# Kernel optimization log

Hardware: AMD Instinct MI355X
Metric: run time of the kernel (lower is better)

## Reference

```python
import jax, jax.numpy as jnp
import numpy as np

N = 100000   # nodes
E = 1600000  # edges
IN, HID, OUT = 128, 256, 64


def _glorot(key, shape):
    fan_in, fan_out = shape[1], shape[0]
    lim = (6.0 / (fan_in + fan_out)) ** 0.5
    return jax.random.uniform(key, shape, jnp.float32, -lim, lim)


def setup_inputs() -> dict:
    key = jax.random.key(0)
    ks = jax.random.split(key, 8)
    x = jax.random.normal(ks[0], (N, IN), jnp.float32)
    edge_index = jax.random.randint(ks[1], (2, E), 0, N, jnp.int64)
    # SAGEConv params: lin_l (neighbor path, has bias), lin_r (root path, no bias)
    return {
        "x": x,
        "edge_index": edge_index,
        "W1_l": _glorot(ks[2], (HID, IN)),
        "b1": jnp.zeros((HID,), jnp.float32),
        "W1_r": _glorot(ks[3], (HID, IN)),
        "W2_l": _glorot(ks[4], (OUT, HID)),
        "b2": jnp.zeros((OUT,), jnp.float32),
        "W2_r": _glorot(ks[5], (OUT, HID)),
    }


def _sage_conv(x, src, dst, W_l, b, W_r):
    # mean aggregation of neighbor features at destination nodes
    msg = x[src]                                             # [E, d] gather
    agg = jax.ops.segment_sum(msg, dst, num_segments=N)      # [N, d]
    cnt = jax.ops.segment_sum(jnp.ones((src.shape[0],), jnp.float32), dst,
                              num_segments=N)                # [N]
    mean = agg / jnp.maximum(cnt, 1.0)[:, None]
    return mean @ W_l.T + b + x @ W_r.T


def reference(x, edge_index, W1_l, b1, W1_r, W2_l, b2, W2_r):
    src, dst = edge_index[0], edge_index[1]
    h = jax.nn.relu(_sage_conv(x, src, dst, W1_l, b1, W1_r))
    # dropout is identity in eval mode
    return _sage_conv(h, src, dst, W2_l, b2, W2_r)
```

## Files before the change

### kernel.cpp

```cpp
#include <hip/hip_runtime.h>
#include <hip/hip_bf16.h>

#define NNODE 100000
#define NEDGE 1600000
#define NBBLK 512
#define CHUNK (NEDGE / NBBLK)
#define NB2 ((NNODE + 1023) >> 10)

typedef __attribute__((ext_vector_type(8))) short bf16x8;
typedef __attribute__((ext_vector_type(4))) float f32x4;

__device__ __forceinline__ unsigned short f2bf(float f){
  unsigned u = __float_as_uint(f);
  u += 0x7fffu + ((u >> 16) & 1u);
  return (unsigned short)(u >> 16);
}
__device__ __forceinline__ unsigned pk2(float a, float b){
  return (unsigned)f2bf(a) | ((unsigned)f2bf(b) << 16);
}
__device__ __forceinline__ float bflo(unsigned v){ return __uint_as_float(v << 16); }
__device__ __forceinline__ float bfhi(unsigned v){ return __uint_as_float(v & 0xffff0000u); }

__global__ __launch_bounds__(256) void k_hist(const int* __restrict__ dst,
                                              unsigned* __restrict__ gh){
  __shared__ unsigned h[NB2];
  for (int t = threadIdx.x; t < NB2; t += 256) h[t] = 0;
  __syncthreads();
  int base = blockIdx.x * CHUNK;
  for (int j = threadIdx.x; j < CHUNK; j += 256)
    atomicAdd(&h[dst[base + j] >> 10], 1u);
  __syncthreads();
  for (int t = threadIdx.x; t < NB2; t += 256) gh[blockIdx.x * NB2 + t] = h[t];
}

__global__ __launch_bounds__(512) void k_scan512(const unsigned* __restrict__ gh,
                                                 unsigned* __restrict__ gbase,
                                                 unsigned* __restrict__ btot){
  int b = blockIdx.x, t = threadIdx.x;
  int lane = t & 63, wv = t >> 6;
  unsigned v = gh[t * NB2 + b];
  unsigned s = v;
  #pragma unroll
  for (int off = 1; off < 64; off <<= 1){
    unsigned u = __shfl_up(s, off, 64);
    if (lane >= off) s += u;
  }
  __shared__ unsigned wsum[8];
  if (lane == 63) wsum[wv] = s;
  __syncthreads();
  unsigned woff = 0;
  for (int w = 0; w < wv; ++w) woff += wsum[w];
  gbase[t * NB2 + b] = woff + s - v;
  if (t == 511) btot[b] = woff + s;
}

__global__ __launch_bounds__(128) void k_scanb(const unsigned* __restrict__ btot,
                                               unsigned* __restrict__ bbase,
                                               unsigned* __restrict__ rowptr){
  __shared__ unsigned buf[128];
  int tid = threadIdx.x;
  unsigned v = (tid < NB2) ? btot[tid] : 0u;
  buf[tid] = v;
  __syncthreads();
  #pragma unroll
  for (int off = 1; off < 128; off <<= 1){
    unsigned t = (tid >= off) ? buf[tid - off] : 0u;
    __syncthreads();
    buf[tid] += t;
    __syncthreads();
  }
  if (tid < NB2) bbase[tid] = buf[tid] - v;
  if (tid == 0){ bbase[NB2] = NEDGE; rowptr[NNODE] = NEDGE; }
}

__global__ __launch_bounds__(256) void k_binscat(const int* __restrict__ src,
                                                 const int* __restrict__ dst,
                                                 const unsigned* __restrict__ gbase,
                                                 const unsigned* __restrict__ bbase,
                                                 unsigned* __restrict__ pairs){
  __shared__ unsigned cur[NB2];
  for (int t = threadIdx.x; t < NB2; t += 256)
    cur[t] = bbase[t] + gbase[blockIdx.x * NB2 + t];
  __syncthreads();
  int base = blockIdx.x * CHUNK;
  for (int j = threadIdx.x; j < CHUNK; j += 256){
    int s = src[base + j], d = dst[base + j];
    unsigned p = atomicAdd(&cur[d >> 10], 1u);
    pairs[p] = ((unsigned)s << 10) | (unsigned)(d & 1023);
  }
}

__global__ __launch_bounds__(1024) void k_buildcsr(const unsigned* __restrict__ bbase,
                                                   const unsigned* __restrict__ pairs,
                                                   unsigned* __restrict__ rowptr,
                                                   unsigned* __restrict__ col){
  __shared__ unsigned hist[1024];
  __shared__ unsigned wsum[16];
  const int b = blockIdx.x, tid = threadIdx.x;
  const int lane = tid & 63, wv = tid >> 6;
  const unsigned e0 = bbase[b], e1 = bbase[b + 1];
  const int nb0 = b << 10;
  hist[tid] = 0;
  __syncthreads();
  for (unsigned j = e0 + tid; j < e1; j += 1024)
    atomicAdd(&hist[pairs[j] & 1023u], 1u);
  __syncthreads();
  unsigned v = hist[tid];
  unsigned s = v;
  #pragma unroll
  for (int off = 1; off < 64; off <<= 1){
    unsigned u = __shfl_up(s, off, 64);
    if (lane >= off) s += u;
  }
  if (lane == 63) wsum[wv] = s;
  __syncthreads();
  unsigned woff = 0;
  for (int w = 0; w < wv; ++w) woff += wsum[w];
  unsigned gpos = e0 + woff + s - v;
  if (nb0 + tid < NNODE) rowptr[nb0 + tid] = gpos;
  __syncthreads();
  hist[tid] = gpos;
  __syncthreads();
  for (unsigned j = e0 + tid; j < e1; j += 1024){
    unsigned e = pairs[j];
    unsigned p = atomicAdd(&hist[e & 1023u], 1u);
    col[p] = e >> 10;
  }
}

__global__ void k_xcvt(const float* __restrict__ x, unsigned* __restrict__ A1u){
  int i = blockIdx.x * 256 + threadIdx.x;
  if (i >= NNODE * 32) return;
  float4 v = ((const float4*)x)[i];
  int e = i * 4;
  int row = e >> 7, c = e & 127;
  unsigned* d = A1u + (size_t)row * 128 + 64 + (c >> 1);
  d[0] = pk2(v.x, v.y);
  d[1] = pk2(v.z, v.w);
}

__global__ void k_wcvt1(const float* __restrict__ W1l, const float* __restrict__ W1r,
                        unsigned short* __restrict__ Bwt1){
  int i = blockIdx.x * 256 + threadIdx.x;
  if (i >= 256 * 256) return;
  int n = i >> 8, k = i & 255;
  float v = (k < 128) ? W1l[n * 128 + k] : W1r[n * 128 + (k - 128)];
  Bwt1[i] = f2bf(v);
}

__global__ void k_wcvt2(const float* __restrict__ W2l, const float* __restrict__ W2r,
                        unsigned short* __restrict__ Bwt2){
  int i = blockIdx.x * 256 + threadIdx.x;
  if (i >= 128 * 256) return;
  int n = i >> 8, k = i & 255;
  float v = (n < 64) ? W2l[n * 256 + k] : W2r[(n - 64) * 256 + k];
  Bwt2[i] = f2bf(v);
}

__global__ __launch_bounds__(256) void k_agg1(const unsigned* __restrict__ rowptr,
                                              const unsigned* __restrict__ col,
                                              unsigned* __restrict__ A1u){
  int gw = (blockIdx.x * 256 + threadIdx.x) >> 6;
  int lane = threadIdx.x & 63;
  if (gw >= NNODE) return;
  unsigned s0 = rowptr[gw], s1 = rowptr[gw + 1];
  float ax = 0.f, ay = 0.f;
  unsigned j = s0;
  for (; j + 3 < s1; j += 4){
    unsigned c0 = col[j], c1 = col[j+1], c2 = col[j+2], c3 = col[j+3];
    unsigned v0 = A1u[(size_t)c0 * 128 + 64 + lane];
    unsigned v1 = A1u[(size_t)c1 * 128 + 64 + lane];
    unsigned v2 = A1u[(size_t)c2 * 128 + 64 + lane];
    unsigned v3 = A1u[(size_t)c3 * 128 + 64 + lane];
    ax += bflo(v0) + bflo(v1) + bflo(v2) + bflo(v3);
    ay += bfhi(v0) + bfhi(v1) + bfhi(v2) + bfhi(v3);
  }
  for (; j < s1; ++j){
    unsigned v = A1u[(size_t)col[j] * 128 + 64 + lane];
    ax += bflo(v); ay += bfhi(v);
  }
  float inv = 1.f / fmaxf((float)(s1 - s0), 1.f);
  A1u[(size_t)gw * 128 + lane] = pk2(ax * inv, ay * inv);
}

template<int BN, bool RELU, bool BIAS>
__global__ __launch_bounds__(256) void k_gemm(const unsigned short* __restrict__ A,
                                              const unsigned short* __restrict__ B,
                                              const float* __restrict__ bias,
                                              unsigned short* __restrict__ C,
                                              int nrows){
  constexpr int NF = BN / 64;
  __shared__ unsigned short a_t[64 * 64];
  __shared__ unsigned short b_t[BN * 64];
  const int tid = threadIdx.x, wave = tid >> 6, lane = tid & 63;
  const int row0 = blockIdx.x * 64;
  char* ab = (char*)a_t;
  char* bb = (char*)b_t;

  f32x4 acc[4][NF];
  #pragma unroll
  for (int m = 0; m < 4; ++m)
    #pragma unroll
    for (int n = 0; n < NF; ++n)
      acc[m][n] = (f32x4){0.f, 0.f, 0.f, 0.f};

  for (int kt = 0; kt < 4; ++kt){
    {
      int r = tid >> 2;
      int gr = row0 + r; if (gr > nrows - 1) gr = nrows - 1;
      const uint4* s4 = (const uint4*)(A + (size_t)gr * 256 + kt * 64);
      int c0 = (tid & 3) * 2;
      uint4 v0 = s4[c0], v1 = s4[c0 + 1];
      *(uint4*)(ab + r * 128 + ((c0 * 16) ^ ((r & 7) << 4))) = v0;
      *(uint4*)(ab + r * 128 + (((c0 + 1) * 16) ^ ((r & 7) << 4))) = v1;
    }
    {
      constexpr int CPT = BN / 32;
      #pragma unroll
      for (int c = 0; c < CPT; ++c){
        int gc = tid * CPT + c;
        int n = gc >> 3, ck = gc & 7;
        uint4 v = ((const uint4*)(B + (size_t)n * 256 + kt * 64))[ck];
        *(uint4*)(bb + n * 128 + ((ck * 16) ^ ((n & 7) << 4))) = v;
      }
    }
    __syncthreads();
    #pragma unroll
    for (int kk = 0; kk < 2; ++kk){
      int k2 = (kk * 32 + ((lane >> 4) * 8)) * 2;
      bf16x8 af[4];
      #pragma unroll
      for (int m = 0; m < 4; ++m){
        int rr = m * 16 + (lane & 15);
        af[m] = *(const bf16x8*)(ab + rr * 128 + (k2 ^ ((rr & 7) << 4)));
      }
      #pragma unroll
      for (int n = 0; n < NF; ++n){
        int cc = wave * (16 * NF) + n * 16 + (lane & 15);
        bf16x8 bfv = *(const bf16x8*)(bb + cc * 128 + (k2 ^ ((cc & 7) << 4)));
        #pragma unroll
        for (int m = 0; m < 4; ++m)
          acc[m][n] = __builtin_amdgcn_mfma_f32_16x16x32_bf16(af[m], bfv, acc[m][n], 0, 0, 0);
      }
    }
    __syncthreads();
  }
  #pragma unroll
  for (int m = 0; m < 4; ++m){
    int rbase = row0 + m * 16 + ((lane >> 4) << 2);
    #pragma unroll
    for (int r = 0; r < 4; ++r){
      if (rbase + r < nrows){
        #pragma unroll
        for (int n = 0; n < NF; ++n){
          int cc = wave * (16 * NF) + n * 16 + (lane & 15);
          float v = acc[m][n][r];
          if (BIAS) v += bias[cc];
          if (RELU) v = fmaxf(v, 0.f);
          C[(size_t)(rbase + r) * BN + cc] = f2bf(v);
        }
      }
    }
  }
}

__global__ __launch_bounds__(256) void k_agg2(const unsigned* __restrict__ rowptr,
                                              const unsigned* __restrict__ col,
                                              const unsigned short* __restrict__ zr,
                                              const float* __restrict__ b2,
                                              float* __restrict__ out){
  int t = blockIdx.x * 256 + threadIdx.x;
  int node = t >> 4, gl = t & 15;
  if (node >= NNODE) return;
  unsigned s0 = rowptr[node], s1 = rowptr[node + 1];
  float a0 = 0.f, a1 = 0.f, a2 = 0.f, a3 = 0.f;
  unsigned j = s0;
  for (; j + 3 < s1; j += 4){
    unsigned c0 = col[j], c1 = col[j+1], c2 = col[j+2], c3 = col[j+3];
    uint2 v0 = *(const uint2*)(zr + (size_t)c0 * 128 + gl * 4);
    uint2 v1 = *(const uint2*)(zr + (size_t)c1 * 128 + gl * 4);
    uint2 v2 = *(const uint2*)(zr + (size_t)c2 * 128 + gl * 4);
    uint2 v3 = *(const uint2*)(zr + (size_t)c3 * 128 + gl * 4);
    a0 += bflo(v0.x) + bflo(v1.x) + bflo(v2.x) + bflo(v3.x);
    a1 += bfhi(v0.x) + bfhi(v1.x) + bfhi(v2.x) + bfhi(v3.x);
    a2 += bflo(v0.y) + bflo(v1.y) + bflo(v2.y) + bflo(v3.y);
    a3 += bfhi(v0.y) + bfhi(v1.y) + bfhi(v2.y) + bfhi(v3.y);
  }
  for (; j < s1; ++j){
    uint2 v = *(const uint2*)(zr + (size_t)col[j] * 128 + gl * 4);
    a0 += bflo(v.x); a1 += bfhi(v.x); a2 += bflo(v.y); a3 += bfhi(v.y);
  }
  float inv = 1.f / fmaxf((float)(s1 - s0), 1.f);
  uint2 rv = *(const uint2*)(zr + (size_t)node * 128 + 64 + gl * 4);
  float4 res;
  res.x = a0 * inv + bflo(rv.x) + b2[gl * 4 + 0];
  res.y = a1 * inv + bfhi(rv.x) + b2[gl * 4 + 1];
  res.z = a2 * inv + bflo(rv.y) + b2[gl * 4 + 2];
  res.w = a3 * inv + bfhi(rv.y) + b2[gl * 4 + 3];
  ((float4*)out)[(size_t)node * 16 + gl] = res;
}

extern "C" void kernel_launch(void* const* d_in, const int* in_sizes, int n_in,
                              void* d_out, int out_size, void* d_ws, size_t ws_size,
                              hipStream_t stream) {
  const float* x   = (const float*)d_in[0];
  const int*   ei  = (const int*)d_in[1];
  const float* W1l = (const float*)d_in[2];
  const float* b1  = (const float*)d_in[3];
  const float* W1r = (const float*)d_in[4];
  const float* W2l = (const float*)d_in[5];
  const float* b2  = (const float*)d_in[6];
  const float* W2r = (const float*)d_in[7];
  float* out = (float*)d_out;

  char* ws = (char*)d_ws;
  size_t off = 0;
  auto alloc = [&](size_t bytes) -> void* {
    void* p = ws + off;
    off = (off + bytes + 255) & ~(size_t)255;
    return p;
  };
  unsigned* rowptr = (unsigned*)alloc((size_t)(NNODE + 1) * 4);
  unsigned* col    = (unsigned*)alloc((size_t)NEDGE * 4);
  unsigned* pairs  = (unsigned*)alloc((size_t)NEDGE * 4);
  unsigned* gh     = (unsigned*)alloc((size_t)NBBLK * NB2 * 4);
  unsigned* gbase  = (unsigned*)alloc((size_t)NBBLK * NB2 * 4);
  unsigned* btot   = (unsigned*)alloc((size_t)NB2 * 4);
  unsigned* bbase  = (unsigned*)alloc((size_t)(NB2 + 1) * 4);
  unsigned short* A1   = (unsigned short*)alloc((size_t)NNODE * 256 * 2);
  unsigned short* h    = (unsigned short*)alloc((size_t)NNODE * 256 * 2);
  unsigned short* zr   = (unsigned short*)alloc((size_t)NNODE * 128 * 2);
  unsigned short* Bwt1 = (unsigned short*)alloc(256 * 256 * 2);
  unsigned short* Bwt2 = (unsigned short*)alloc(128 * 256 * 2);

  const int* srcv = ei;
  const int* dstv = ei + NEDGE;

  k_hist<<<NBBLK, 256, 0, stream>>>(dstv, gh);
  k_scan512<<<NB2, 512, 0, stream>>>(gh, gbase, btot);
  k_scanb<<<1, 128, 0, stream>>>(btot, bbase, rowptr);
  k_binscat<<<NBBLK, 256, 0, stream>>>(srcv, dstv, gbase, bbase, pairs);
  k_buildcsr<<<NB2, 1024, 0, stream>>>(bbase, pairs, rowptr, col);

  k_xcvt<<<(NNODE * 32 + 255) / 256, 256, 0, stream>>>(x, (unsigned*)A1);
  k_wcvt1<<<256, 256, 0, stream>>>(W1l, W1r, Bwt1);
  k_wcvt2<<<128, 256, 0, stream>>>(W2l, W2r, Bwt2);

  k_agg1<<<(NNODE + 3) / 4, 256, 0, stream>>>(rowptr, col, (unsigned*)A1);

  int gblocks = (NNODE + 63) / 64;
  k_gemm<256, true,  true ><<<gblocks, 256, 0, stream>>>(A1, Bwt1, b1, h, NNODE);
  k_gemm<128, false, false><<<gblocks, 256, 0, stream>>>(h,  Bwt2, nullptr, zr, NNODE);

  k_agg2<<<(NNODE * 16 + 255) / 256, 256, 0, stream>>>(rowptr, col, zr, b2, out);
}
```

Measured before the change: 330.8 us.

## Gather neighbor features as fp8 copies and restructure aggregation lanes

Makes extra fp8 (e4m3) copies of x and of the layer-2 neighbor projection, and has both aggregation kernels gather these instead of bf16 rows. This halves the bytes per gathered row. Each wavefront now processes four edges in parallel using 16-lane groups and combines the partial sums with cross-lane shuffles. The cost is an additional conversion kernel and write for z, plus a large loss of precision in the aggregated features, which may exceed the tolerance.

Result: no change. 324.8 us (-1.8%).

```diff
diff --git a/kernel.cpp b/kernel.cpp
--- a/kernel.cpp
+++ b/kernel.cpp
@@ -9,6 +9,7 @@
 
 typedef __attribute__((ext_vector_type(8))) short bf16x8;
 typedef __attribute__((ext_vector_type(4))) float f32x4;
+typedef __attribute__((ext_vector_type(2))) float f32x2;
 
 __device__ __forceinline__ unsigned short f2bf(float f){
   unsigned u = __float_as_uint(f);
@@ -128,7 +129,8 @@
   }
 }
 
-__global__ void k_xcvt(const float* __restrict__ x, unsigned* __restrict__ A1u){
+__global__ void k_xcvt(const float* __restrict__ x, unsigned* __restrict__ A1u,
+                       unsigned* __restrict__ x8u){
   int i = blockIdx.x * 256 + threadIdx.x;
   if (i >= NNODE * 32) return;
   float4 v = ((const float4*)x)[i];
@@ -137,6 +139,9 @@
   unsigned* d = A1u + (size_t)row * 128 + 64 + (c >> 1);
   d[0] = pk2(v.x, v.y);
   d[1] = pk2(v.z, v.w);
+  unsigned p = (unsigned)__builtin_amdgcn_cvt_pk_fp8_f32(v.x, v.y, 0, false);
+  p = (unsigned)__builtin_amdgcn_cvt_pk_fp8_f32(v.z, v.w, (int)p, true);
+  x8u[(size_t)row * 32 + (c >> 2)] = p;
 }
 
 __global__ void k_wcvt1(const float* __restrict__ W1l, const float* __restrict__ W1r,
@@ -157,30 +162,78 @@
   Bwt2[i] = f2bf(v);
 }
 
+__global__ void k_zcvt(const unsigned* __restrict__ zru, unsigned* __restrict__ z8u){
+  int i = blockIdx.x * 256 + threadIdx.x;
+  if (i >= NNODE * 16) return;
+  int node = i >> 4, g = i & 15;
+  uint2 v = ((const uint2*)(zru + (size_t)node * 64))[g];
+  unsigned p = (unsigned)__builtin_amdgcn_cvt_pk_fp8_f32(bflo(v.x), bfhi(v.x), 0, false);
+  p = (unsigned)__builtin_amdgcn_cvt_pk_fp8_f32(bflo(v.y), bfhi(v.y), (int)p, true);
+  z8u[(size_t)node * 16 + g] = p;
+}
+
 __global__ __launch_bounds__(256) void k_agg1(const unsigned* __restrict__ rowptr,
                                               const unsigned* __restrict__ col,
+                                              const unsigned* __restrict__ x8u,
                                               unsigned* __restrict__ A1u){
   int gw = (blockIdx.x * 256 + threadIdx.x) >> 6;
   int lane = threadIdx.x & 63;
   if (gw >= NNODE) return;
   unsigned s0 = rowptr[gw], s1 = rowptr[gw + 1];
-  float ax = 0.f, ay = 0.f;
+  const int sel = lane >> 4, u = lane & 15;
+  const uint2* x82 = (const uint2*)x8u;
+  float a0=0.f,a1=0.f,a2=0.f,a3=0.f,a4=0.f,a5=0.f,a6=0.f,a7=0.f;
   unsigned j = s0;
+  for (; j + 7 < s1; j += 8){
+    unsigned ca = col[j + sel], cb = col[j + 4 + sel];
+    uint2 va = x82[(size_t)ca * 16 + u];
+    uint2 vb = x82[(size_t)cb * 16 + u];
+    f32x2 p;
+    p = __builtin_amdgcn_cvt_pk_f32_fp8((int)va.x, false); a0+=p.x; a1+=p.y;
+    p = __builtin_amdgcn_cvt_pk_f32_fp8((int)va.x, true ); a2+=p.x; a3+=p.y;
+    p = __builtin_amdgcn_cvt_pk_f32_fp8((int)va.y, false); a4+=p.x; a5+=p.y;
+    p = __builtin_amdgcn_cvt_pk_f32_fp8((int)va.y, true ); a6+=p.x; a7+=p.y;
+    p = __builtin_amdgcn_cvt_pk_f32_fp8((int)vb.x, false); a0+=p.x; a1+=p.y;
+    p = __builtin_amdgcn_cvt_pk_f32_fp8((int)vb.x, true ); a2+=p.x; a3+=p.y;
+    p = __builtin_amdgcn_cvt_pk_f32_fp8((int)vb.y, false); a4+=p.x; a5+=p.y;
+    p = __builtin_amdgcn_cvt_pk_f32_fp8((int)vb.y, true ); a6+=p.x; a7+=p.y;
+  }
   for (; j + 3 < s1; j += 4){
-    unsigned c0 = col[j], c1 = col[j+1], c2 = col[j+2], c3 = col[j+3];
-    unsigned v0 = A1u[(size_t)c0 * 128 + 64 + lane];
-    unsigned v1 = A1u[(size_t)c1 * 128 + 64 + lane];
-    unsigned v2 = A1u[(size_t)c2 * 128 + 64 + lane];
-    unsigned v3 = A1u[(size_t)c3 * 128 + 64 + lane];
-    ax += bflo(v0) + bflo(v1) + bflo(v2) + bflo(v3);
-    ay += bfhi(v0) + bfhi(v1) + bfhi(v2) + bfhi(v3);
-  }
-  for (; j < s1; ++j){
-    unsigned v = A1u[(size_t)col[j] * 128 + 64 + lane];
-    ax += bflo(v); ay += bfhi(v);
-  }
-  float inv = 1.f / fmaxf((float)(s1 - s0), 1.f);
-  A1u[(size_t)gw * 128 + lane] = pk2(ax * inv, ay * inv);
+    unsigned ca = col[j + sel];
+    uint2 va = x82[(size_t)ca * 16 + u];
+    f32x2 p;
+    p = __builtin_amdgcn_cvt_pk_f32_fp8((int)va.x, false); a0+=p.x; a1+=p.y;
+    p = __builtin_amdgcn_cvt_pk_f32_fp8((int)va.x, true ); a2+=p.x; a3+=p.y;
+    p = __builtin_amdgcn_cvt_pk_f32_fp8((int)va.y, false); a4+=p.x; a5+=p.y;
+    p = __builtin_amdgcn_cvt_pk_f32_fp8((int)va.y, true ); a6+=p.x; a7+=p.y;
+  }
+  int rem = (int)(s1 - j);
+  if (sel < rem){
+    unsigned ca = col[j + sel];
+    uint2 va = x82[(size_t)ca * 16 + u];
+    f32x2 p;
+    p = __builtin_amdgcn_cvt_pk_f32_fp8((int)va.x, false); a0+=p.x; a1+=p.y;
+    p = __builtin_amdgcn_cvt_pk_f32_fp8((int)va.x, true ); a2+=p.x; a3+=p.y;
+    p = __builtin_amdgcn_cvt_pk_f32_fp8((int)va.y, false); a4+=p.x; a5+=p.y;
+    p = __builtin_amdgcn_cvt_pk_f32_fp8((int)va.y, true ); a6+=p.x; a7+=p.y;
+  }
+  a0 += __shfl_xor(a0, 16, 64); a1 += __shfl_xor(a1, 16, 64);
+  a2 += __shfl_xor(a2, 16, 64); a3 += __shfl_xor(a3, 16, 64);
+  a4 += __shfl_xor(a4, 16, 64); a5 += __shfl_xor(a5, 16, 64);
+  a6 += __shfl_xor(a6, 16, 64); a7 += __shfl_xor(a7, 16, 64);
+  a0 += __shfl_xor(a0, 32, 64); a1 += __shfl_xor(a1, 32, 64);
+  a2 += __shfl_xor(a2, 32, 64); a3 += __shfl_xor(a3, 32, 64);
+  a4 += __shfl_xor(a4, 32, 64); a5 += __shfl_xor(a5, 32, 64);
+  a6 += __shfl_xor(a6, 32, 64); a7 += __shfl_xor(a7, 32, 64);
+  if (lane < 16){
+    float inv = 1.f / fmaxf((float)(s1 - s0), 1.f);
+    uint4 w;
+    w.x = pk2(a0 * inv, a1 * inv);
+    w.y = pk2(a2 * inv, a3 * inv);
+    w.z = pk2(a4 * inv, a5 * inv);
+    w.w = pk2(a6 * inv, a7 * inv);
+    *(uint4*)(A1u + (size_t)gw * 128 + 4 * lane) = w;
+  }
 }
 
 template<int BN, bool RELU, bool BIAS>
@@ -266,38 +319,57 @@
 
 __global__ __launch_bounds__(256) void k_agg2(const unsigned* __restrict__ rowptr,
                                               const unsigned* __restrict__ col,
-                                              const unsigned short* __restrict__ zr,
+                                              const unsigned* __restrict__ z8u,
+                                              const unsigned* __restrict__ zru,
                                               const float* __restrict__ b2,
                                               float* __restrict__ out){
-  int t = blockIdx.x * 256 + threadIdx.x;
-  int node = t >> 4, gl = t & 15;
-  if (node >= NNODE) return;
-  unsigned s0 = rowptr[node], s1 = rowptr[node + 1];
-  float a0 = 0.f, a1 = 0.f, a2 = 0.f, a3 = 0.f;
+  int gw = (blockIdx.x * 256 + threadIdx.x) >> 6;
+  int lane = threadIdx.x & 63;
+  if (gw >= NNODE) return;
+  unsigned s0 = rowptr[gw], s1 = rowptr[gw + 1];
+  const int sel = lane >> 4, u = lane & 15;
+  float a0=0.f,a1=0.f,a2=0.f,a3=0.f;
   unsigned j = s0;
+  for (; j + 7 < s1; j += 8){
+    unsigned ca = col[j + sel], cb = col[j + 4 + sel];
+    unsigned va = z8u[(size_t)ca * 16 + u];
+    unsigned vb = z8u[(size_t)cb * 16 + u];
+    f32x2 p;
+    p = __builtin_amdgcn_cvt_pk_f32_fp8((int)va, false); a0+=p.x; a1+=p.y;
+    p = __builtin_amdgcn_cvt_pk_f32_fp8((int)va, true ); a2+=p.x; a3+=p.y;
+    p = __builtin_amdgcn_cvt_pk_f32_fp8((int)vb, false); a0+=p.x; a1+=p.y;
+    p = __builtin_amdgcn_cvt_pk_f32_fp8((int)vb, true ); a2+=p.x; a3+=p.y;
+  }
   for (; j + 3 < s1; j += 4){
-    unsigned c0 = col[j], c1 = col[j+1], c2 = col[j+2], c3 = col[j+3];
-    uint2 v0 = *(const uint2*)(zr + (size_t)c0 * 128 + gl * 4);
-    uint2 v1 = *(const uint2*)(zr + (size_t)c1 * 128 + gl * 4);
-    uint2 v2 = *(const uint2*)(zr + (size_t)c2 * 128 + gl * 4);
-    uint2 v3 = *(const uint2*)(zr + (size_t)c3 * 128 + gl * 4);
-    a0 += bflo(v0.x) + bflo(v1.x) + bflo(v2.x) + bflo(v3.x);
-    a1 += bfhi(v0.x) + bfhi(v1.x) + bfhi(v2.x) + bfhi(v3.x);
-    a2 += bflo(v0.y) + bflo(v1.y) + bflo(v2.y) + bflo(v3.y);
-    a3 += bfhi(v0.y) + bfhi(v1.y) + bfhi(v2.y) + bfhi(v3.y);
-  }
-  for (; j < s1; ++j){
-    uint2 v = *(const uint2*)(zr + (size_t)col[j] * 128 + gl * 4);
-    a0 += bflo(v.x); a1 += bfhi(v.x); a2 += bflo(v.y); a3 += bfhi(v.y);
-  }
-  float inv = 1.f / fmaxf((float)(s1 - s0), 1.f);
-  uint2 rv = *(const uint2*)(zr + (size_t)node * 128 + 64 + gl * 4);
-  float4 res;
-  res.x = a0 * inv + bflo(rv.x) + b2[gl * 4 + 0];
-  res.y = a1 * inv + bfhi(rv.x) + b2[gl * 4 + 1];
-  res.z = a2 * inv + bflo(rv.y) + b2[gl * 4 + 2];
-  res.w = a3 * inv + bfhi(rv.y) + b2[gl * 4 + 3];
-  ((float4*)out)[(size_t)node * 16 + gl] = res;
+    unsigned ca = col[j + sel];
+    unsigned va = z8u[(size_t)ca * 16 + u];
+    f32x2 p;
+    p = __builtin_amdgcn_cvt_pk_f32_fp8((int)va, false); a0+=p.x; a1+=p.y;
+    p = __builtin_amdgcn_cvt_pk_f32_fp8((int)va, true ); a2+=p.x; a3+=p.y;
+  }
+  int rem = (int)(s1 - j);
+  if (sel < rem){
+    unsigned ca = col[j + sel];
+    unsigned va = z8u[(size_t)ca * 16 + u];
+    f32x2 p;
+    p = __builtin_amdgcn_cvt_pk_f32_fp8((int)va, false); a0+=p.x; a1+=p.y;
+    p = __builtin_amdgcn_cvt_pk_f32_fp8((int)va, true ); a2+=p.x; a3+=p.y;
+  }
+  a0 += __shfl_xor(a0, 16, 64); a1 += __shfl_xor(a1, 16, 64);
+  a2 += __shfl_xor(a2, 16, 64); a3 += __shfl_xor(a3, 16, 64);
+  a0 += __shfl_xor(a0, 32, 64); a1 += __shfl_xor(a1, 32, 64);
+  a2 += __shfl_xor(a2, 32, 64); a3 += __shfl_xor(a3, 32, 64);
+  if (lane < 16){
+    float inv = 1.f / fmaxf((float)(s1 - s0), 1.f);
+    uint2 rv = ((const uint2*)(zru + (size_t)gw * 64 + 32))[lane];
+    float4 bv = ((const float4*)b2)[lane];
+    float4 res;
+    res.x = a0 * inv + bflo(rv.x) + bv.x;
+    res.y = a1 * inv + bfhi(rv.x) + bv.y;
+    res.z = a2 * inv + bflo(rv.y) + bv.z;
+    res.w = a3 * inv + bfhi(rv.y) + bv.w;
+    ((float4*)out)[(size_t)gw * 16 + lane] = res;
+  }
 }
 
 extern "C" void kernel_launch(void* const* d_in, const int* in_sizes, int n_in,
@@ -330,6 +402,8 @@
   unsigned short* A1   = (unsigned short*)alloc((size_t)NNODE * 256 * 2);
   unsigned short* h    = (unsigned short*)alloc((size_t)NNODE * 256 * 2);
   unsigned short* zr   = (unsigned short*)alloc((size_t)NNODE * 128 * 2);
+  unsigned* x8u        = (unsigned*)alloc((size_t)NNODE * 32 * 4);
+  unsigned* z8u        = (unsigned*)alloc((size_t)NNODE * 16 * 4);
   unsigned short* Bwt1 = (unsigned short*)alloc(256 * 256 * 2);
   unsigned short* Bwt2 = (unsigned short*)alloc(128 * 256 * 2);
 
@@ -342,15 +416,16 @@
   k_binscat<<<NBBLK, 256, 0, stream>>>(srcv, dstv, gbase, bbase, pairs);
   k_buildcsr<<<NB2, 1024, 0, stream>>>(bbase, pairs, rowptr, col);
 
-  k_xcvt<<<(NNODE * 32 + 255) / 256, 256, 0, stream>>>(x, (unsigned*)A1);
+  k_xcvt<<<(NNODE * 32 + 255) / 256, 256, 0, stream>>>(x, (unsigned*)A1, x8u);
   k_wcvt1<<<256, 256, 0, stream>>>(W1l, W1r, Bwt1);
   k_wcvt2<<<128, 256, 0, stream>>>(W2l, W2r, Bwt2);
 
-  k_agg1<<<(NNODE + 3) / 4, 256, 0, stream>>>(rowptr, col, (unsigned*)A1);
+  k_agg1<<<(NNODE + 3) / 4, 256, 0, stream>>>(rowptr, col, x8u, (unsigned*)A1);
 
   int gblocks = (NNODE + 63) / 64;
   k_gemm<256, true,  true ><<<gblocks, 256, 0, stream>>>(A1, Bwt1, b1, h, NNODE);
   k_gemm<128, false, false><<<gblocks, 256, 0, stream>>>(h,  Bwt2, nullptr, zr, NNODE);
 
-  k_agg2<<<(NNODE * 16 + 255) / 256, 256, 0, stream>>>(rowptr, col, zr, b2, out);
-}
+  k_zcvt<<<(NNODE * 16 + 255) / 256, 256, 0, stream>>>((const unsigned*)zr, z8u);
+  k_agg2<<<(NNODE + 3) / 4, 256, 0, stream>>>(rowptr, col, z8u, (const unsigned*)zr, b2, out);
+}
```

## Gather neighbor features in FP8 with multi-edge-per-wave aggregation and fused launches

Applied to the files above, without the earlier changes.

Writes an FP8 copy of x and of the neighbor-path projection z, so both aggregation kernels gather half as many bytes per edge as with bf16. Each wave now processes 8 edges at once with wide vector loads and reduces across lanes with shuffles. Separately, the histogram and x conversion are fused into one launch and the two weight conversions into another. FP8 storage of gathered features adds quantization error, which may threaten tolerance.

New measurement: 318.7 us. -3.6%, faster.

```diff
diff --git a/kernel.cpp b/kernel.cpp
--- a/kernel.cpp
+++ b/kernel.cpp
@@ -9,6 +9,7 @@
 
 typedef __attribute__((ext_vector_type(8))) short bf16x8;
 typedef __attribute__((ext_vector_type(4))) float f32x4;
+typedef __attribute__((ext_vector_type(2))) float f32x2;
 
 __device__ __forceinline__ unsigned short f2bf(float f){
   unsigned u = __float_as_uint(f);
@@ -21,16 +22,34 @@
 __device__ __forceinline__ float bflo(unsigned v){ return __uint_as_float(v << 16); }
 __device__ __forceinline__ float bfhi(unsigned v){ return __uint_as_float(v & 0xffff0000u); }
 
-__global__ __launch_bounds__(256) void k_hist(const int* __restrict__ dst,
-                                              unsigned* __restrict__ gh){
-  __shared__ unsigned h[NB2];
-  for (int t = threadIdx.x; t < NB2; t += 256) h[t] = 0;
-  __syncthreads();
-  int base = blockIdx.x * CHUNK;
-  for (int j = threadIdx.x; j < CHUNK; j += 256)
-    atomicAdd(&h[dst[base + j] >> 10], 1u);
-  __syncthreads();
-  for (int t = threadIdx.x; t < NB2; t += 256) gh[blockIdx.x * NB2 + t] = h[t];
+__global__ __launch_bounds__(256) void k_xh(const float* __restrict__ x,
+                                            unsigned* __restrict__ A1u,
+                                            unsigned* __restrict__ x8u,
+                                            const int* __restrict__ dst,
+                                            unsigned* __restrict__ gh){
+  int bid = blockIdx.x;
+  if (bid < NBBLK){
+    __shared__ unsigned h[NB2];
+    for (int t = threadIdx.x; t < NB2; t += 256) h[t] = 0;
+    __syncthreads();
+    int base = bid * CHUNK;
+    for (int j = threadIdx.x; j < CHUNK; j += 256)
+      atomicAdd(&h[dst[base + j] >> 10], 1u);
+    __syncthreads();
+    for (int t = threadIdx.x; t < NB2; t += 256) gh[bid * NB2 + t] = h[t];
+    return;
+  }
+  int i = (bid - NBBLK) * 256 + threadIdx.x;
+  if (i >= NNODE * 32) return;
+  float4 v = ((const float4*)x)[i];
+  int e = i * 4;
+  int row = e >> 7, c = e & 127;
+  unsigned* d = A1u + (size_t)row * 128 + 64 + (c >> 1);
+  d[0] = pk2(v.x, v.y);
+  d[1] = pk2(v.z, v.w);
+  unsigned p = (unsigned)__builtin_amdgcn_cvt_pk_fp8_f32(v.x, v.y, 0, false);
+  p = (unsigned)__builtin_amdgcn_cvt_pk_fp8_f32(v.z, v.w, (int)p, true);
+  x8u[(size_t)row * 32 + (c >> 2)] = p;
 }
 
 __global__ __launch_bounds__(512) void k_scan512(const unsigned* __restrict__ gh,
@@ -128,66 +147,95 @@
   }
 }
 
-__global__ void k_xcvt(const float* __restrict__ x, unsigned* __restrict__ A1u){
+__global__ void k_wcvt(const float* __restrict__ W1l, const float* __restrict__ W1r,
+                       const float* __restrict__ W2l, const float* __restrict__ W2r,
+                       unsigned short* __restrict__ Bwt1, unsigned short* __restrict__ Bwt2){
   int i = blockIdx.x * 256 + threadIdx.x;
-  if (i >= NNODE * 32) return;
-  float4 v = ((const float4*)x)[i];
-  int e = i * 4;
-  int row = e >> 7, c = e & 127;
-  unsigned* d = A1u + (size_t)row * 128 + 64 + (c >> 1);
-  d[0] = pk2(v.x, v.y);
-  d[1] = pk2(v.z, v.w);
-}
-
-__global__ void k_wcvt1(const float* __restrict__ W1l, const float* __restrict__ W1r,
-                        unsigned short* __restrict__ Bwt1){
-  int i = blockIdx.x * 256 + threadIdx.x;
-  if (i >= 256 * 256) return;
-  int n = i >> 8, k = i & 255;
-  float v = (k < 128) ? W1l[n * 128 + k] : W1r[n * 128 + (k - 128)];
-  Bwt1[i] = f2bf(v);
-}
-
-__global__ void k_wcvt2(const float* __restrict__ W2l, const float* __restrict__ W2r,
-                        unsigned short* __restrict__ Bwt2){
-  int i = blockIdx.x * 256 + threadIdx.x;
-  if (i >= 128 * 256) return;
-  int n = i >> 8, k = i & 255;
-  float v = (n < 64) ? W2l[n * 256 + k] : W2r[(n - 64) * 256 + k];
-  Bwt2[i] = f2bf(v);
+  if (i < 256 * 256){
+    int n = i >> 8, k = i & 255;
+    float v = (k < 128) ? W1l[n * 128 + k] : W1r[n * 128 + (k - 128)];
+    Bwt1[i] = f2bf(v);
+  }
+  int i2 = i - 256 * 256;
+  if (i2 >= 0 && i2 < 128 * 256){
+    int n = i2 >> 8, k = i2 & 255;
+    float v = (n < 64) ? W2l[n * 256 + k] : W2r[(n - 64) * 256 + k];
+    Bwt2[i2] = f2bf(v);
+  }
 }
 
 __global__ __launch_bounds__(256) void k_agg1(const unsigned* __restrict__ rowptr,
                                               const unsigned* __restrict__ col,
+                                              const unsigned* __restrict__ x8u,
                                               unsigned* __restrict__ A1u){
   int gw = (blockIdx.x * 256 + threadIdx.x) >> 6;
   int lane = threadIdx.x & 63;
   if (gw >= NNODE) return;
   unsigned s0 = rowptr[gw], s1 = rowptr[gw + 1];
-  float ax = 0.f, ay = 0.f;
+  const int sel = lane >> 3, u = lane & 7;
+  const uint4* x84 = (const uint4*)x8u;
+  f32x2 A0={0,0},A1={0,0},A2={0,0},A3={0,0},A4={0,0},A5={0,0},A6={0,0},A7={0,0};
   unsigned j = s0;
-  for (; j + 3 < s1; j += 4){
-    unsigned c0 = col[j], c1 = col[j+1], c2 = col[j+2], c3 = col[j+3];
-    unsigned v0 = A1u[(size_t)c0 * 128 + 64 + lane];
-    unsigned v1 = A1u[(size_t)c1 * 128 + 64 + lane];
-    unsigned v2 = A1u[(size_t)c2 * 128 + 64 + lane];
-    unsigned v3 = A1u[(size_t)c3 * 128 + 64 + lane];
-    ax += bflo(v0) + bflo(v1) + bflo(v2) + bflo(v3);
-    ay += bfhi(v0) + bfhi(v1) + bfhi(v2) + bfhi(v3);
-  }
-  for (; j < s1; ++j){
-    unsigned v = A1u[(size_t)col[j] * 128 + 64 + lane];
-    ax += bflo(v); ay += bfhi(v);
-  }
-  float inv = 1.f / fmaxf((float)(s1 - s0), 1.f);
-  A1u[(size_t)gw * 128 + lane] = pk2(ax * inv, ay * inv);
-}
-
-template<int BN, bool RELU, bool BIAS>
+  for (; j + 7 < s1; j += 8){
+    unsigned ca = col[j + sel];
+    uint4 va = x84[(size_t)ca * 8 + u];
+    A0 += __builtin_amdgcn_cvt_pk_f32_fp8((int)va.x, false);
+    A1 += __builtin_amdgcn_cvt_pk_f32_fp8((int)va.x, true );
+    A2 += __builtin_amdgcn_cvt_pk_f32_fp8((int)va.y, false);
+    A3 += __builtin_amdgcn_cvt_pk_f32_fp8((int)va.y, true );
+    A4 += __builtin_amdgcn_cvt_pk_f32_fp8((int)va.z, false);
+    A5 += __builtin_amdgcn_cvt_pk_f32_fp8((int)va.z, true );
+    A6 += __builtin_amdgcn_cvt_pk_f32_fp8((int)va.w, false);
+    A7 += __builtin_amdgcn_cvt_pk_f32_fp8((int)va.w, true );
+  }
+  int rem = (int)(s1 - j);
+  if (sel < rem){
+    unsigned ca = col[j + sel];
+    uint4 va = x84[(size_t)ca * 8 + u];
+    A0 += __builtin_amdgcn_cvt_pk_f32_fp8((int)va.x, false);
+    A1 += __builtin_amdgcn_cvt_pk_f32_fp8((int)va.x, true );
+    A2 += __builtin_amdgcn_cvt_pk_f32_fp8((int)va.y, false);
+    A3 += __builtin_amdgcn_cvt_pk_f32_fp8((int)va.y, true );
+    A4 += __builtin_amdgcn_cvt_pk_f32_fp8((int)va.z, false);
+    A5 += __builtin_amdgcn_cvt_pk_f32_fp8((int)va.z, true );
+    A6 += __builtin_amdgcn_cvt_pk_f32_fp8((int)va.w, false);
+    A7 += __builtin_amdgcn_cvt_pk_f32_fp8((int)va.w, true );
+  }
+  #pragma unroll
+  for (int mask = 8; mask <= 32; mask <<= 1){
+    A0.x += __shfl_xor(A0.x, mask, 64); A0.y += __shfl_xor(A0.y, mask, 64);
+    A1.x += __shfl_xor(A1.x, mask, 64); A1.y += __shfl_xor(A1.y, mask, 64);
+    A2.x += __shfl_xor(A2.x, mask, 64); A2.y += __shfl_xor(A2.y, mask, 64);
+    A3.x += __shfl_xor(A3.x, mask, 64); A3.y += __shfl_xor(A3.y, mask, 64);
+    A4.x += __shfl_xor(A4.x, mask, 64); A4.y += __shfl_xor(A4.y, mask, 64);
+    A5.x += __shfl_xor(A5.x, mask, 64); A5.y += __shfl_xor(A5.y, mask, 64);
+    A6.x += __shfl_xor(A6.x, mask, 64); A6.y += __shfl_xor(A6.y, mask, 64);
+    A7.x += __shfl_xor(A7.x, mask, 64); A7.y += __shfl_xor(A7.y, mask, 64);
+  }
+  if (lane < 8){
+    float inv = 1.f / fmaxf((float)(s1 - s0), 1.f);
+    uint4 w0, w1;
+    w0.x = pk2(A0.x * inv, A0.y * inv);
+    w0.y = pk2(A1.x * inv, A1.y * inv);
+    w0.z = pk2(A2.x * inv, A2.y * inv);
+    w0.w = pk2(A3.x * inv, A3.y * inv);
+    w1.x = pk2(A4.x * inv, A4.y * inv);
+    w1.y = pk2(A5.x * inv, A5.y * inv);
+    w1.z = pk2(A6.x * inv, A6.y * inv);
+    w1.w = pk2(A7.x * inv, A7.y * inv);
+    unsigned* d = A1u + (size_t)gw * 128 + 8 * lane;
+    *(uint4*)d = w0;
+    *(uint4*)(d + 4) = w1;
+  }
+}
+
+template<int BN, bool RELU, bool BIAS, int MODE>
 __global__ __launch_bounds__(256) void k_gemm(const unsigned short* __restrict__ A,
                                               const unsigned short* __restrict__ B,
                                               const float* __restrict__ bias,
                                               unsigned short* __restrict__ C,
+                                              unsigned char* __restrict__ z8,
+                                              unsigned short* __restrict__ r16,
                                               int nrows){
   constexpr int NF = BN / 64;
   __shared__ unsigned short a_t[64 * 64];
@@ -257,7 +305,15 @@
           float v = acc[m][n][r];
           if (BIAS) v += bias[cc];
           if (RELU) v = fmaxf(v, 0.f);
-          C[(size_t)(rbase + r) * BN + cc] = f2bf(v);
+          if (MODE == 0){
+            C[(size_t)(rbase + r) * BN + cc] = f2bf(v);
+          } else {
+            if (cc < 64)
+              z8[(size_t)(rbase + r) * 64 + cc] =
+                (unsigned char)__builtin_amdgcn_cvt_pk_fp8_f32(v, v, 0, false);
+            else
+              r16[(size_t)(rbase + r) * 64 + (cc - 64)] = f2bf(v);
+          }
         }
       }
     }
@@ -266,38 +322,59 @@
 
 __global__ __launch_bounds__(256) void k_agg2(const unsigned* __restrict__ rowptr,
                                               const unsigned* __restrict__ col,
-                                              const unsigned short* __restrict__ zr,
+                                              const unsigned* __restrict__ z8u,
+                                              const unsigned* __restrict__ r16u,
                                               const float* __restrict__ b2,
                                               float* __restrict__ out){
-  int t = blockIdx.x * 256 + threadIdx.x;
-  int node = t >> 4, gl = t & 15;
-  if (node >= NNODE) return;
-  unsigned s0 = rowptr[node], s1 = rowptr[node + 1];
-  float a0 = 0.f, a1 = 0.f, a2 = 0.f, a3 = 0.f;
+  int gw = (blockIdx.x * 256 + threadIdx.x) >> 6;
+  int lane = threadIdx.x & 63;
+  if (gw >= NNODE) return;
+  unsigned s0 = rowptr[gw], s1 = rowptr[gw + 1];
+  const int sel = lane >> 3, u = lane & 7;
+  const uint2* z82 = (const uint2*)z8u;
+  f32x2 A0={0,0},A1={0,0},A2={0,0},A3={0,0};
   unsigned j = s0;
-  for (; j + 3 < s1; j += 4){
-    unsigned c0 = col[j], c1 = col[j+1], c2 = col[j+2], c3 = col[j+3];
-    uint2 v0 = *(const uint2*)(zr + (size_t)c0 * 128 + gl * 4);
-    uint2 v1 = *(const uint2*)(zr + (size_t)c1 * 128 + gl * 4);
-    uint2 v2 = *(const uint2*)(zr + (size_t)c2 * 128 + gl * 4);
-    uint2 v3 = *(const uint2*)(zr + (size_t)c3 * 128 + gl * 4);
-    a0 += bflo(v0.x) + bflo(v1.x) + bflo(v2.x) + bflo(v3.x);
-    a1 += bfhi(v0.x) + bfhi(v1.x) + bfhi(v2.x) + bfhi(v3.x);
-    a2 += bflo(v0.y) + bflo(v1.y) + bflo(v2.y) + bflo(v3.y);
-    a3 += bfhi(v0.y) + bfhi(v1.y) + bfhi(v2.y) + bfhi(v3.y);
-  }
-  for (; j < s1; ++j){
-    uint2 v = *(const uint2*)(zr + (size_t)col[j] * 128 + gl * 4);
-    a0 += bflo(v.x); a1 += bfhi(v.x); a2 += bflo(v.y); a3 += bfhi(v.y);
-  }
-  float inv = 1.f / fmaxf((float)(s1 - s0), 1.f);
-  uint2 rv = *(const uint2*)(zr + (size_t)node * 128 + 64 + gl * 4);
-  float4 res;
-  res.x = a0 * inv + bflo(rv.x) + b2[gl * 4 + 0];
-  res.y = a1 * inv + bfhi(rv.x) + b2[gl * 4 + 1];
-  res.z = a2 * inv + bflo(rv.y) + b2[gl * 4 + 2];
-  res.w = a3 * inv + bfhi(rv.y) + b2[gl * 4 + 3];
-  ((float4*)out)[(size_t)node * 16 + gl] = res;
+  for (; j + 7 < s1; j += 8){
+    unsigned ca = col[j + sel];
+    uint2 va = z82[(size_t)ca * 8 + u];
+    A0 += __builtin_amdgcn_cvt_pk_f32_fp8((int)va.x, false);
+    A1 += __builtin_amdgcn_cvt_pk_f32_fp8((int)va.x, true );
+    A2 += __builtin_amdgcn_cvt_pk_f32_fp8((int)va.y, false);
+    A3 += __builtin_amdgcn_cvt_pk_f32_fp8((int)va.y, true );
+  }
+  int rem = (int)(s1 - j);
+  if (sel < rem){
+    unsigned ca = col[j + sel];
+    uint2 va = z82[(size_t)ca * 8 + u];
+    A0 += __builtin_amdgcn_cvt_pk_f32_fp8((int)va.x, false);
+    A1 += __builtin_amdgcn_cvt_pk_f32_fp8((int)va.x, true );
+    A2 += __builtin_amdgcn_cvt_pk_f32_fp8((int)va.y, false);
+    A3 += __builtin_amdgcn_cvt_pk_f32_fp8((int)va.y, true );
+  }
+  #pragma unroll
+  for (int mask = 8; mask <= 32; mask <<= 1){
+    A0.x += __shfl_xor(A0.x, mask, 64); A0.y += __shfl_xor(A0.y, mask, 64);
+    A1.x += __shfl_xor(A1.x, mask, 64); A1.y += __shfl_xor(A1.y, mask, 64);
+    A2.x += __shfl_xor(A2.x, mask, 64); A2.y += __shfl_xor(A2.y, mask, 64);
+    A3.x += __shfl_xor(A3.x, mask, 64); A3.y += __shfl_xor(A3.y, mask, 64);
+  }
+  if (lane < 8){
+    float inv = 1.f / fmaxf((float)(s1 - s0), 1.f);
+    uint4 rv = ((const uint4*)(r16u + (size_t)gw * 32))[lane];
+    float4 b0 = ((const float4*)b2)[2 * lane];
+    float4 b1 = ((const float4*)b2)[2 * lane + 1];
+    float4 o0, o1;
+    o0.x = A0.x * inv + bflo(rv.x) + b0.x;
+    o0.y = A0.y * inv + bfhi(rv.x) + b0.y;
+    o0.z = A1.x * inv + bflo(rv.y) + b0.z;
+    o0.w = A1.y * inv + bfhi(rv.y) + b0.w;
+    o1.x = A2.x * inv + bflo(rv.z) + b1.x;
+    o1.y = A2.y * inv + bfhi(rv.z) + b1.y;
+    o1.z = A3.x * inv + bflo(rv.w) + b1.z;
+    o1.w = A3.y * inv + bfhi(rv.w) + b1.w;
+    ((float4*)out)[(size_t)gw * 16 + 2 * lane] = o0;
+    ((float4*)out)[(size_t)gw * 16 + 2 * lane + 1] = o1;
+  }
 }
 
 extern "C" void kernel_launch(void* const* d_in, const int* in_sizes, int n_in,
@@ -329,28 +406,28 @@
   unsigned* bbase  = (unsigned*)alloc((size_t)(NB2 + 1) * 4);
   unsigned short* A1   = (unsigned short*)alloc((size_t)NNODE * 256 * 2);
   unsigned short* h    = (unsigned short*)alloc((size_t)NNODE * 256 * 2);
-  unsigned short* zr   = (unsigned short*)alloc((size_t)NNODE * 128 * 2);
+  unsigned short* r16  = (unsigned short*)alloc((size_t)NNODE * 64 * 2);
+  unsigned* x8u        = (unsigned*)alloc((size_t)NNODE * 32 * 4);
+  unsigned char* z8    = (unsigned char*)alloc((size_t)NNODE * 64);
   unsigned short* Bwt1 = (unsigned short*)alloc(256 * 256 * 2);
   unsigned short* Bwt2 = (unsigned short*)alloc(128 * 256 * 2);
 
   const int* srcv = ei;
   const int* dstv = ei + NEDGE;
 
-  k_hist<<<NBBLK, 256, 0, stream>>>(dstv, gh);
+  k_xh<<<NBBLK + (NNODE * 32 + 255) / 256, 256, 0, stream>>>(x, (unsigned*)A1, x8u, dstv, gh);
   k_scan512<<<NB2, 512, 0, stream>>>(gh, gbase, btot);
   k_scanb<<<1, 128, 0, stream>>>(btot, bbase, rowptr);
   k_binscat<<<NBBLK, 256, 0, stream>>>(srcv, dstv, gbase, bbase, pairs);
   k_buildcsr<<<NB2, 1024, 0, stream>>>(bbase, pairs, rowptr, col);
 
-  k_xcvt<<<(NNODE * 32 + 255) / 256, 256, 0, stream>>>(x, (unsigned*)A1);
-  k_wcvt1<<<256, 256, 0, stream>>>(W1l, W1r, Bwt1);
-  k_wcvt2<<<128, 256, 0, stream>>>(W2l, W2r, Bwt2);
-
-  k_agg1<<<(NNODE + 3) / 4, 256, 0, stream>>>(rowptr, col, (unsigned*)A1);
+  k_wcvt<<<(256 * 256 + 128 * 256 + 255) / 256, 256, 0, stream>>>(W1l, W1r, W2l, W2r, Bwt1, Bwt2);
+
+  k_agg1<<<(NNODE + 3) / 4, 256, 0, stream>>>(rowptr, col, x8u, (unsigned*)A1);
 
   int gblocks = (NNODE + 63) / 64;
-  k_gemm<256, true,  true ><<<gblocks, 256, 0, stream>>>(A1, Bwt1, b1, h, NNODE);
-  k_gemm<128, false, false><<<gblocks, 256, 0, stream>>>(h,  Bwt2, nullptr, zr, NNODE);
-
-  k_agg2<<<(NNODE * 16 + 255) / 256, 256, 0, stream>>>(rowptr, col, zr, b2, out);
-}
+  k_gemm<256, true,  true,  0><<<gblocks, 256, 0, stream>>>(A1, Bwt1, b1, h, nullptr, nullptr, NNODE);
+  k_gemm<128, false, false, 2><<<gblocks, 256, 0, stream>>>(h,  Bwt2, nullptr, nullptr, z8, r16, NNODE);
+
+  k_agg2<<<(NNODE + 3) / 4, 256, 0, stream>>>(rowptr, col, (const unsigned*)z8, (const unsigned*)r16, b2, out);
+}
```
